# Performance work log

Measured on AMD Instinct MI355X. Metric: run time of the kernel, lower is better.

## Reference

```python
import jax, jax.numpy as jnp
import numpy as np

S_GRID = 14.0
L_COORD = 5.0
L_NOOBJ = 0.5
B = 2


def _xywh2xyxy(b):
    # b: [..., 4] with (x, y, w, h); x,y are divided by S per the original module
    xy = b[..., :2] / S_GRID
    wh = b[..., 2:4]
    return jnp.concatenate([xy - 0.5 * wh, xy + 0.5 * wh], axis=-1)


def setup_inputs() -> dict:
    key = jax.random.key(0)
    k1, k2, k3, k4 = jax.random.split(key, 4)
    N, S, C = 4096, 14, 20
    pred_tensor = jax.random.uniform(k1, (N, S, S, B * 5 + C), dtype=jnp.float32, minval=0.05, maxval=1.0)
    target_boxes = jax.random.uniform(k2, (N, S, S, 4), dtype=jnp.float32, minval=0.05, maxval=1.0)
    target_cls = jax.random.normal(k3, (N, S, S, C), dtype=jnp.float32)
    has_object_map = jax.random.randint(k4, (N, S, S), 0, 2).astype(jnp.bool_)
    return {"pred_tensor": pred_tensor, "target_boxes": target_boxes,
            "target_cls": target_cls, "has_object_map": has_object_map}


def reference(pred_tensor, target_boxes, target_cls, has_object_map):
    N = pred_tensor.shape[0]
    mask = has_object_map                      # [N,S,S] bool
    maskf = mask.astype(pred_tensor.dtype)
    pb = pred_tensor[..., :B * 5].reshape(*pred_tensor.shape[:3], B, 5)  # [N,S,S,B,5]
    pc = pred_tensor[..., B * 5:]              # [N,S,S,20]

    # class loss: masked sum of squared errors over classes
    cls_loss = jnp.sum(maskf * jnp.sum((target_cls - pc) ** 2, axis=-1))

    # no-object loss: conf^2 on cells without objects, summed over both boxes
    conf = pb[..., 4]                          # [N,S,S,B]
    no_obj_loss = L_NOOBJ * jnp.sum(jnp.where(~mask[..., None], conf, 0.0) ** 2)

    # per-cell IoU of target vs each of the B predicted boxes (diag of original NxM)
    t_xyxy = _xywh2xyxy(target_boxes)          # [N,S,S,4]
    p_xyxy = _xywh2xyxy(pb[..., :4])           # [N,S,S,B,4]
    lt = jnp.maximum(t_xyxy[..., None, :2], p_xyxy[..., :2])
    rb = jnp.minimum(t_xyxy[..., None, 2:], p_xyxy[..., 2:])
    wh = jnp.clip(rb - lt, 0.0)
    inter = wh[..., 0] * wh[..., 1]            # [N,S,S,B]
    area_t = (t_xyxy[..., 2] - t_xyxy[..., 0]) * (t_xyxy[..., 3] - t_xyxy[..., 1])
    area_p = (p_xyxy[..., 2] - p_xyxy[..., 0]) * (p_xyxy[..., 3] - p_xyxy[..., 1])
    iou = inter / (area_t[..., None] + area_p - inter)  # [N,S,S,B]

    best_iou = jnp.max(iou, axis=-1)           # [N,S,S]
    best_idx = jnp.argmax(iou, axis=-1)        # [N,S,S]
    best_box = jnp.take_along_axis(pb, best_idx[..., None, None], axis=3)[..., 0, :]  # [N,S,S,5]

    xy_diff = jnp.where(mask[..., None], best_box[..., :2] - target_boxes[..., :2], 0.0)
    wh_p = jnp.where(mask[..., None], best_box[..., 2:4], 1.0)
    wh_t = jnp.where(mask[..., None], target_boxes[..., 2:4], 1.0)
    reg_loss = L_COORD * (jnp.sum(xy_diff ** 2)
                          + jnp.sum((jnp.sqrt(wh_p) - jnp.sqrt(wh_t)) ** 2))

    # containing-object confidence loss: mse(best_iou, best_box_conf) on object cells
    containing_obj_loss = jnp.sum(jnp.where(mask, best_iou - best_box[..., 4], 0.0) ** 2)

    total_loss = (cls_loss + no_obj_loss + reg_loss + containing_obj_loss) / N
    return (total_loss, reg_loss, containing_obj_loss, no_obj_loss, cls_loss)
```

## Files before the change

### kernel.cpp

```cpp
#include <hip/hip_runtime.h>
#include <math.h>


#define BLOCK 256
#define WPB 4
#define CPW 64

__global__ __launch_bounds__(BLOCK) void k_yolo(
    const float*  __restrict__ pred,
    const float4* __restrict__ tbox4,
    const float4* __restrict__ tcls4,
    const int*    __restrict__ mask,
    float4*       __restrict__ partial,
    int n_cells)
{
    __shared__ float  sp[WPB][CPW * 30];
    __shared__ float4 swr[WPB];
    const int tid  = threadIdx.x;
    const int lane = tid & 63;
    const int w    = tid >> 6;
    const long long cell0 = ((long long)blockIdx.x * WPB + w) * CPW;
    const long long base = (cell0 < (long long)n_cells) ? cell0
                         : (long long)n_cells - CPW;
    const int remc = (int)(((long long)n_cells - base) < CPW
                           ? ((long long)n_cells - base) : CPW);
    const int lim4 = (remc * 30) >> 2;
    const int lim5 = remc * 5;

    const bool  vf  = (cell0 + (long long)lane) < (long long)n_cells;
    const float vff = vf ? 1.0f : 0.0f;
    const int   li  = (lane < remc) ? lane : (remc - 1);

    const float4* p4 = reinterpret_cast<const float4*>(pred + base * 30);
    float4* s4 = reinterpret_cast<float4*>(sp[w]);
    int   mraw = mask[base + li];
    float4 tb  = tbox4[base + li];
    #pragma unroll
    for (int i = 0; i < 8; ++i) {
        int k = lane + i * 64;
        k = (k < lim4) ? k : (lim4 - 1);
        s4[k] = p4[k];
    }
    const int   mflag = vf ? mraw : 0;
    const float mff   = (float)mflag;

    __syncthreads();

    float cls = 0.f, noobj, reg, cont;
    {
        const float2* pc2 = reinterpret_cast<const float2*>(sp[w] + lane * 30);
        float2 v0 = pc2[0], v1 = pc2[1], v2 = pc2[2], v3 = pc2[3], v4 = pc2[4];
        float txc = tb.x / 14.0f, tyc = tb.y / 14.0f;
        float t0 = txc - 0.5f * tb.z, t1 = tyc - 0.5f * tb.w;
        float t2 = txc + 0.5f * tb.z, t3 = tyc + 0.5f * tb.w;
        float area_t = (t2 - t0) * (t3 - t1);
        float bx[2] = { v0.x, v2.y }, by[2] = { v0.y, v3.x };
        float bw[2] = { v1.x, v3.y }, bh[2] = { v1.y, v4.x };
        float bcf[2] = { v2.x, v4.y };
        float iou[2];
        #pragma unroll
        for (int b = 0; b < 2; ++b) {
            float px = bx[b] / 14.0f, py = by[b] / 14.0f;
            float q0 = px - 0.5f * bw[b], q1 = py - 0.5f * bh[b];
            float q2 = px + 0.5f * bw[b], q3 = py + 0.5f * bh[b];
            float lt0 = fmaxf(t0, q0), lt1 = fmaxf(t1, q1);
            float rb0 = fminf(t2, q2), rb1 = fminf(t3, q3);
            float ww = fmaxf(rb0 - lt0, 0.f), hh = fmaxf(rb1 - lt1, 0.f);
            float inter = ww * hh;
            float area_p = (q2 - q0) * (q3 - q1);
            iou[b] = inter / (area_t + area_p - inter);
        }
        int bi = (iou[1] > iou[0]) ? 1 : 0;
        float dx = bx[bi] - tb.x, dy = by[bi] - tb.y;
        float swd = sqrtf(bw[bi]) - sqrtf(tb.z);
        float shd = sqrtf(bh[bi]) - sqrtf(tb.w);
        reg  = mff * 5.0f * (dx*dx + dy*dy + swd*swd + shd*shd);
        float dco = iou[bi] - bcf[bi];
        cont = mff * dco * dco;
        noobj = (vff - mff) * 0.5f * (v2.x * v2.x + v4.y * v4.y);
    }

    {
        const float4* t4 = tcls4 + base * 5;
        float4 t[5];
        float2 a[5], b2[5];
        float  mc[5];
        #pragma unroll
        for (int i = 0; i < 5; ++i) {
            int j = lane + i * 64;
            int jc = (j < lim5) ? j : (lim5 - 1);
            t[i] = t4[jc];
            int c = j / 5;
            int q = j - 5 * c;
            int m = __shfl(mflag, c, 64);
            mc[i] = (j < lim5) ? (float)m : 0.0f;
            const float2* s2 = reinterpret_cast<const float2*>(sp[w] + c * 30 + 10 + q * 4);
            a[i]  = s2[0];
            b2[i] = s2[1];
        }
        #pragma unroll
        for (int i = 0; i < 5; ++i) {
            float d0 = t[i].x - a[i].x,  d1 = t[i].y - a[i].y;
            float d2 = t[i].z - b2[i].x, d3 = t[i].w - b2[i].y;
            cls += mc[i] * (d0*d0 + d1*d1 + d2*d2 + d3*d3);
        }
    }

    #pragma unroll
    for (int off = 32; off; off >>= 1) {
        cls   += __shfl_down(cls,   off, 64);
        noobj += __shfl_down(noobj, off, 64);
        reg   += __shfl_down(reg,   off, 64);
        cont  += __shfl_down(cont,  off, 64);
    }
    if (lane == 0) swr[w] = make_float4(cls, noobj, reg, cont);
    __syncthreads();
    if (tid == 0) {
        float4 a = swr[0];
        #pragma unroll
        for (int i = 1; i < WPB; ++i) {
            float4 b = swr[i];
            a.x += b.x; a.y += b.y; a.z += b.z; a.w += b.w;
        }
        partial[blockIdx.x] = a;
    }
}

__global__ __launch_bounds__(BLOCK) void k_final(
    const float4* __restrict__ partial, int nblocks,
    float* __restrict__ out, float invN)
{
    float4 acc = make_float4(0.f, 0.f, 0.f, 0.f);
    for (int b = threadIdx.x; b < nblocks; b += BLOCK) {
        float4 v = partial[b];
        acc.x += v.x; acc.y += v.y; acc.z += v.z; acc.w += v.w;
    }
    #pragma unroll
    for (int off = 32; off; off >>= 1) {
        acc.x += __shfl_down(acc.x, off, 64);
        acc.y += __shfl_down(acc.y, off, 64);
        acc.z += __shfl_down(acc.z, off, 64);
        acc.w += __shfl_down(acc.w, off, 64);
    }
    __shared__ float4 sw[WPB];
    int lane = threadIdx.x & 63, w = threadIdx.x >> 6;
    if (lane == 0) sw[w] = acc;
    __syncthreads();
    if (threadIdx.x == 0) {
        float cls = 0.f, noobj = 0.f, reg = 0.f, cont = 0.f;
        #pragma unroll
        for (int i = 0; i < WPB; ++i) {
            cls += sw[i].x; noobj += sw[i].y; reg += sw[i].z; cont += sw[i].w;
        }
        out[0] = (cls + noobj + reg + cont) * invN;
        out[1] = reg;
        out[2] = cont;
        out[3] = noobj;
        out[4] = cls;
    }
}

extern "C" void kernel_launch(void* const* d_in, const int* in_sizes, int n_in,
                              void* d_out, int out_size, void* d_ws, size_t ws_size,
                              hipStream_t stream) {
    const float*  pred  = (const float*)d_in[0];
    const float4* tbox4 = (const float4*)d_in[1];
    const float4* tcls4 = (const float4*)d_in[2];
    const int*    mask  = (const int*)d_in[3];
    float* out = (float*)d_out;
    float4* partial = (float4*)d_ws;

    int n_cells = in_sizes[3];
    int N = in_sizes[0] / (14 * 14 * 30);
    int nblocks = (n_cells + BLOCK - 1) / BLOCK;

    hipLaunchKernelGGL(k_yolo, dim3(nblocks), dim3(BLOCK), 0, stream,
                       pred, tbox4, tcls4, mask, partial, n_cells);
    hipLaunchKernelGGL(k_final, dim3(1), dim3(BLOCK), 0, stream,
                       partial, nblocks, out, 1.0f / (float)N);
}
```

Before: 203.3 us.

## Load pred tile directly into LDS and replace per-wave sync with waitcnt

Uses global_load_lds to stream each wave's 7680-byte prediction tile straight into LDS, bypassing registers, and issues the class-target loads before waiting. The block-wide __syncthreads is replaced by a vmcnt waitcnt, since each wave only reads its own LDS slice. The per-element mask shuffles become a single ballot plus bit extraction, and launch bounds now request 4 blocks per CU. The risks are hand-written waitcnt encoding and LDS ordering correctness, which depend on ISA details.

```diff
diff --git a/kernel.cpp b/kernel.cpp
--- a/kernel.cpp
+++ b/kernel.cpp
@@ -6,7 +6,10 @@
 #define WPB 4
 #define CPW 64
 
-__global__ __launch_bounds__(BLOCK) void k_yolo(
+typedef __attribute__((address_space(3))) void       lds_void_t;
+typedef __attribute__((address_space(1))) const void gbl_void_t;
+
+__global__ __launch_bounds__(BLOCK, 4) void k_yolo(
     const float*  __restrict__ pred,
     const float4* __restrict__ tbox4,
     const float4* __restrict__ tcls4,
@@ -19,32 +22,49 @@
     const int tid  = threadIdx.x;
     const int lane = tid & 63;
     const int w    = tid >> 6;
+    const long long nc    = n_cells;
     const long long cell0 = ((long long)blockIdx.x * WPB + w) * CPW;
-    const long long base = (cell0 < (long long)n_cells) ? cell0
-                         : (long long)n_cells - CPW;
-    const int remc = (int)(((long long)n_cells - base) < CPW
-                           ? ((long long)n_cells - base) : CPW);
-    const int lim4 = (remc * 30) >> 2;
+    const long long base  = (cell0 < nc) ? cell0 : (nc - CPW);
+    const int remc = (int)(((nc - base) < CPW) ? (nc - base) : CPW);
     const int lim5 = remc * 5;
+    const int li   = (lane < remc) ? lane : (remc - 1);
 
-    const bool  vf  = (cell0 + (long long)lane) < (long long)n_cells;
-    const float vff = vf ? 1.0f : 0.0f;
-    const int   li  = (lane < remc) ? lane : (remc - 1);
+    const char* gb   = (const char*)pred + base * 120;
+    const char* gend = (const char*)pred + nc * 120 - 16;
+    char* lb = (char*)&sp[w][0];
+    #pragma unroll
+    for (int i = 0; i < 7; ++i) {
+        const char* ga = gb + i * 1024 + lane * 16;
+        if (ga > gend) ga = gend;
+        __builtin_amdgcn_global_load_lds((gbl_void_t*)ga,
+                                         (lds_void_t*)(lb + i * 1024), 16, 0, 0);
+    }
+    if (lane < 32) {
+        const char* ga = gb + 7168 + lane * 16;
+        if (ga > gend) ga = gend;
+        __builtin_amdgcn_global_load_lds((gbl_void_t*)ga,
+                                         (lds_void_t*)(lb + 7168), 16, 0, 0);
+    }
 
-    const float4* p4 = reinterpret_cast<const float4*>(pred + base * 30);
-    float4* s4 = reinterpret_cast<float4*>(sp[w]);
-    int   mraw = mask[base + li];
-    float4 tb  = tbox4[base + li];
+    int    mraw = mask[base + li];
+    float4 tb   = tbox4[base + li];
+    const float4* t4 = tcls4 + base * 5;
+    float4 t[5];
     #pragma unroll
-    for (int i = 0; i < 8; ++i) {
-        int k = lane + i * 64;
-        k = (k < lim4) ? k : (lim4 - 1);
-        s4[k] = p4[k];
+    for (int i = 0; i < 5; ++i) {
+        int j  = lane + i * 64;
+        int jc = (j < lim5) ? j : (lim5 - 1);
+        t[i] = t4[jc];
     }
+
+    __builtin_amdgcn_s_waitcnt(0xF70);
+    __asm__ volatile("" ::: "memory");
+
+    const bool  vf    = (cell0 + (long long)lane) < nc;
     const int   mflag = vf ? mraw : 0;
     const float mff   = (float)mflag;
-
-    __syncthreads();
+    const float vff   = vf ? 1.0f : 0.0f;
+    const unsigned long long mbits = __ballot(mflag != 0);
 
     float cls = 0.f, noobj, reg, cont;
     {
@@ -80,30 +100,18 @@
         noobj = (vff - mff) * 0.5f * (v2.x * v2.x + v4.y * v4.y);
     }
 
-    {
-        const float4* t4 = tcls4 + base * 5;
-        float4 t[5];
-        float2 a[5], b2[5];
-        float  mc[5];
-        #pragma unroll
-        for (int i = 0; i < 5; ++i) {
-            int j = lane + i * 64;
-            int jc = (j < lim5) ? j : (lim5 - 1);
-            t[i] = t4[jc];
-            int c = j / 5;
-            int q = j - 5 * c;
-            int m = __shfl(mflag, c, 64);
-            mc[i] = (j < lim5) ? (float)m : 0.0f;
-            const float2* s2 = reinterpret_cast<const float2*>(sp[w] + c * 30 + 10 + q * 4);
-            a[i]  = s2[0];
-            b2[i] = s2[1];
-        }
-        #pragma unroll
-        for (int i = 0; i < 5; ++i) {
-            float d0 = t[i].x - a[i].x,  d1 = t[i].y - a[i].y;
-            float d2 = t[i].z - b2[i].x, d3 = t[i].w - b2[i].y;
-            cls += mc[i] * (d0*d0 + d1*d1 + d2*d2 + d3*d3);
-        }
+    #pragma unroll
+    for (int i = 0; i < 5; ++i) {
+        int j = lane + i * 64;
+        int c = j / 5;
+        int q = j - 5 * c;
+        float mcf = (float)((int)((mbits >> c) & 1ull));
+        mcf = (j < lim5) ? mcf : 0.0f;
+        const float2* s2 = reinterpret_cast<const float2*>(sp[w] + c * 30 + 10 + q * 4);
+        float2 a = s2[0], b2 = s2[1];
+        float d0 = t[i].x - a.x,  d1 = t[i].y - a.y;
+        float d2 = t[i].z - b2.x, d3 = t[i].w - b2.y;
+        cls += mcf * (d0*d0 + d1*d1 + d2*d2 + d3*d3);
     }
 
     #pragma unroll
```

Result: no change. 203.3 us (-0.0%).
